# Optimization experiments

Hardware: AMD Instinct MI355X
Metric: run time of the kernel (lower is better)

## Reference

```python
import jax, jax.numpy as jnp
import numpy as np

D = 1024
D_PRE_HEAD = 128
H = 16
D_ROPE = D_PRE_HEAD // 2          # 64
DC_V = D_PRE_HEAD                 # 128
DC_KV = D_PRE_HEAD // 8           # 16
DC_Q = D // 4                     # 256
Q_HEAD_DIM = D_PRE_HEAD + D_ROPE  # 192
MEG_D = D_PRE_HEAD + DC_V         # 256
MAX_LEN = 8192
EPS = 1e-7


def rms_norm(x, w):
    x32 = x.astype(jnp.float32)
    var = jnp.mean(x32 * x32, axis=-1, keepdims=True)
    return w * (x32 * jax.lax.rsqrt(var + EPS)).astype(x.dtype)


def rope_cos_sin():
    inv_freq = 1.0 / (10000.0 ** (jnp.arange(0, D_ROPE, 2, dtype=jnp.float32) / D_ROPE))
    freqs = jnp.outer(jnp.arange(MAX_LEN, dtype=jnp.float32), inv_freq)
    emb = jnp.concatenate([freqs, freqs], axis=-1)  # [MAX_LEN, D_ROPE]
    return jnp.cos(emb), jnp.sin(emb)


def rope_reshape(x):
    # view(...,d//2,2).transpose(-1,-2).reshape == concat(even, odd) along last dim
    return jnp.concatenate([x[..., 0::2], x[..., 1::2]], axis=-1)


def rope_rotate(x):
    h = x.shape[-1] // 2
    return jnp.concatenate([-x[..., h:], x[..., :h]], axis=-1)


def setup_inputs() -> dict:
    key = jax.random.key(0)
    ks = jax.random.split(key, 12)
    B, SQ, SKV = 2, 2048, 2048
    s = 0.02
    return {
        "q_inputs": jax.random.normal(ks[0], (B, SQ, D), jnp.float32),
        "kv_input": jax.random.normal(ks[1], (B, SKV, D), jnp.float32),
        "q_pos_ids": jax.random.randint(ks[2], (B, SQ), 0, MAX_LEN),
        "kv_pos_ids": jax.random.randint(ks[3], (B, SKV), 0, MAX_LEN),
        # weights stored as [in, out] (torch Linear weight transposed)
        "Wq_down": jax.random.normal(ks[4], (D, DC_Q), jnp.float32) * s,
        "q_norm_w": jnp.ones((DC_Q,), jnp.float32),
        "Wq_up": jax.random.normal(ks[5], (DC_Q, H * Q_HEAD_DIM), jnp.float32) * s,
        "Wkv_down": jax.random.normal(ks[6], (D, DC_KV + D_ROPE), jnp.float32) * s,
        "kv_norm_w": jnp.ones((DC_KV,), jnp.float32),
        "Wkv_up": jax.random.normal(ks[7], (DC_KV, H * MEG_D), jnp.float32) * s,
        "Wout": jax.random.normal(ks[8], (H * DC_V, D), jnp.float32) * s,
    }


def reference(q_inputs, kv_input, q_pos_ids, kv_pos_ids,
              Wq_down, q_norm_w, Wq_up, Wkv_down, kv_norm_w, Wkv_up, Wout):
    B, SQ, _ = q_inputs.shape
    SKV = kv_input.shape[1]

    # query path: low-rank down -> RMSNorm -> up
    q = rms_norm(q_inputs @ Wq_down, q_norm_w) @ Wq_up
    q = q.reshape(B, SQ, H, Q_HEAD_DIM).transpose(0, 2, 1, 3)  # [B,H,SQ,192]
    q_nope, q_rope = q[..., :D_PRE_HEAD], q[..., D_PRE_HEAD:]

    # kv path: compressed latent + decoupled rope slice
    ckv_full = kv_input @ Wkv_down                              # [B,SKV,DC_KV+D_ROPE]
    c_kv, k_rope = ckv_full[..., :DC_KV], ckv_full[..., DC_KV:]
    c_kv = rms_norm(c_kv, kv_norm_w)
    kv = (c_kv @ Wkv_up).reshape(B, SKV, H, MEG_D).transpose(0, 2, 1, 3)
    k_nope, value = kv[..., :D_PRE_HEAD], kv[..., D_PRE_HEAD:]  # [B,H,SKV,128] each
    k_rope = k_rope[:, None, :, :]                              # [B,1,SKV,64]

    # RoPE with per-token position ids
    cos, sin = rope_cos_sin()
    q_cos, q_sin = cos[q_pos_ids][:, None], sin[q_pos_ids][:, None]   # [B,1,SQ,64]
    k_cos, k_sin = cos[kv_pos_ids][:, None], sin[kv_pos_ids][:, None]
    qr = rope_reshape(q_rope)
    kr = rope_reshape(k_rope)
    q_rope = qr * q_cos + rope_rotate(qr) * q_sin
    k_rope = kr * k_cos + rope_rotate(kr) * k_sin

    query = jnp.concatenate([q_nope, q_rope], axis=-1)                         # [B,H,SQ,192]
    key_t = jnp.concatenate([k_nope, jnp.broadcast_to(k_rope, (B, H, SKV, D_ROPE))], axis=-1)

    scale = 1.0 / jnp.sqrt(jnp.asarray(Q_HEAD_DIM, query.dtype))
    scores = jnp.einsum('bhqd,bhkd->bhqk', query, key_t) * scale
    attn = jax.nn.softmax(scores, axis=-1)
    out = jnp.einsum('bhqk,bhkd->bhqd', attn, value)                           # [B,H,SQ,128]
    out = out.transpose(0, 2, 1, 3).reshape(B, SQ, H * DC_V)
    return out @ Wout
```

## Files before the change

kernel.cpp:

```cpp
#include <hip/hip_runtime.h>

typedef unsigned short u16;
typedef unsigned int u32;
typedef u16 u16x4 __attribute__((ext_vector_type(4)));
typedef u16 u16x8 __attribute__((ext_vector_type(8)));
typedef u32 u32x4 __attribute__((ext_vector_type(4)));
typedef float f32x4 __attribute__((ext_vector_type(4)));
typedef __bf16 bf16x8 __attribute__((ext_vector_type(8)));

#define DEV static __device__ __forceinline__

DEV float bf2f(u16 u) { u32 v = ((u32)u) << 16; float f; __builtin_memcpy(&f, &v, 4); return f; }
DEV u16 f2bf(float f) { u32 v; __builtin_memcpy(&v, &f, 4); v += 0x7fffu + ((v >> 16) & 1u); return (u16)(v >> 16); }
DEV bf16x8 ld_frag(const u16* p) { u16x8 v = *(const u16x8*)p; return __builtin_bit_cast(bf16x8, v); }

#define LOG10000 9.210340372f

__global__ __launch_bounds__(256) void k_wtrans(const float* __restrict__ in, u16* __restrict__ out,
                                                int R, int C, int Rp) {
  __shared__ float tile[32][33];
  int c0 = blockIdx.x * 32, r0 = blockIdx.y * 32;
  int tx = threadIdx.x & 31, ty = threadIdx.x >> 5;
#pragma unroll
  for (int p = 0; p < 4; p++) {
    int r = r0 + ty + p * 8, c = c0 + tx;
    tile[ty + p * 8][tx] = (r < R && c < C) ? in[(size_t)r * C + c] : 0.f;
  }
  __syncthreads();
#pragma unroll
  for (int p = 0; p < 4; p++)
    out[(size_t)(c0 + ty + p * 8) * Rp + r0 + tx] = f2bf(tile[tx][ty + p * 8]);
}

template <int OUT_BF16>
__global__ __launch_bounds__(256) void k_gemm(const u16* __restrict__ A, const u16* __restrict__ Bt,
                                              void* __restrict__ Cv, int M, int N, int K) {
  constexpr int LSTR = 40;
  __shared__ u16 As[128 * LSTR], Bs[128 * LSTR];
  const int tid = threadIdx.x, l = tid & 63, w = tid >> 6;
  const int nwg = gridDim.x * gridDim.y;
  const int lin = blockIdx.y * gridDim.x + blockIdx.x;
  const int swzb = (lin & 7) * (nwg >> 3) + (lin >> 3);
  const int m0 = (swzb / gridDim.x) * 128, n0 = (swzb % gridDim.x) * 128;
  const int wr = (w >> 1) * 64, wc = (w & 1) * 64;
  const int lr = l & 15, lk = (l >> 4) * 8;
  const int sr = tid >> 2, sc = (tid & 3) * 8;
  f32x4 acc[4][4] = {};
  const u16* pa0 = A + (size_t)(m0 + sr) * K + sc;
  const u16* pa1 = A + (size_t)(m0 + 64 + sr) * K + sc;
  const u16* pb0 = Bt + (size_t)(n0 + sr) * K + sc;
  const u16* pb1 = Bt + (size_t)(n0 + 64 + sr) * K + sc;
  u16x8 va0 = *(const u16x8*)pa0, va1 = *(const u16x8*)pa1;
  u16x8 vb0 = *(const u16x8*)pb0, vb1 = *(const u16x8*)pb1;
  for (int k0 = 0; k0 < K; k0 += 32) {
    *(u16x8*)&As[sr * LSTR + sc] = va0;
    *(u16x8*)&As[(64 + sr) * LSTR + sc] = va1;
    *(u16x8*)&Bs[sr * LSTR + sc] = vb0;
    *(u16x8*)&Bs[(64 + sr) * LSTR + sc] = vb1;
    __syncthreads();
    if (k0 + 32 < K) {
      va0 = *(const u16x8*)(pa0 + k0 + 32);
      va1 = *(const u16x8*)(pa1 + k0 + 32);
      vb0 = *(const u16x8*)(pb0 + k0 + 32);
      vb1 = *(const u16x8*)(pb1 + k0 + 32);
    }
    bf16x8 af[4], bf[4];
#pragma unroll
    for (int i = 0; i < 4; i++) af[i] = ld_frag(&As[(wr + i * 16 + lr) * LSTR + lk]);
#pragma unroll
    for (int j = 0; j < 4; j++) bf[j] = ld_frag(&Bs[(wc + j * 16 + lr) * LSTR + lk]);
#pragma unroll
    for (int i = 0; i < 4; i++)
#pragma unroll
      for (int j = 0; j < 4; j++)
        acc[i][j] = __builtin_amdgcn_mfma_f32_16x16x32_bf16(af[i], bf[j], acc[i][j], 0, 0, 0);
    __syncthreads();
  }
#pragma unroll
  for (int i = 0; i < 4; i++)
#pragma unroll
    for (int j = 0; j < 4; j++) {
      int row = m0 + wr + i * 16 + (l >> 4) * 4;
      int col = n0 + wc + j * 16 + lr;
#pragma unroll
      for (int r = 0; r < 4; r++) {
        if (OUT_BF16) ((u16*)Cv)[(size_t)(row + r) * N + col] = f2bf(acc[i][j][r]);
        else          ((float*)Cv)[(size_t)(row + r) * N + col] = acc[i][j][r];
      }
    }
}

template <int OUT_BF16>
__global__ __launch_bounds__(256) void k_gemmh(const u16* __restrict__ A, const u16* __restrict__ Bt,
                                               void* __restrict__ Cv, int M, int N, int K) {
  constexpr int LSTR = 40;
  __shared__ u16 As[64 * LSTR], Bs[128 * LSTR];
  const int tid = threadIdx.x, l = tid & 63, w = tid >> 6;
  const int nwg = gridDim.x * gridDim.y;
  const int lin = blockIdx.y * gridDim.x + blockIdx.x;
  const int swzb = (lin & 7) * (nwg >> 3) + (lin >> 3);
  const int m0 = (swzb / gridDim.x) * 64, n0 = (swzb % gridDim.x) * 128;
  const int wr = (w >> 1) * 32, wc = (w & 1) * 64;
  const int lr = l & 15, lk = (l >> 4) * 8;
  const int sr = tid >> 2, sc = (tid & 3) * 8;
  f32x4 acc[2][4] = {};
  const u16* pa0 = A + (size_t)(m0 + sr) * K + sc;
  const u16* pb0 = Bt + (size_t)(n0 + sr) * K + sc;
  const u16* pb1 = Bt + (size_t)(n0 + 64 + sr) * K + sc;
  u16x8 va0 = *(const u16x8*)pa0;
  u16x8 vb0 = *(const u16x8*)pb0, vb1 = *(const u16x8*)pb1;
  for (int k0 = 0; k0 < K; k0 += 32) {
    *(u16x8*)&As[sr * LSTR + sc] = va0;
    *(u16x8*)&Bs[sr * LSTR + sc] = vb0;
    *(u16x8*)&Bs[(64 + sr) * LSTR + sc] = vb1;
    __syncthreads();
    if (k0 + 32 < K) {
      va0 = *(const u16x8*)(pa0 + k0 + 32);
      vb0 = *(const u16x8*)(pb0 + k0 + 32);
      vb1 = *(const u16x8*)(pb1 + k0 + 32);
    }
    bf16x8 af[2], bf[4];
#pragma unroll
    for (int i = 0; i < 2; i++) af[i] = ld_frag(&As[(wr + i * 16 + lr) * LSTR + lk]);
#pragma unroll
    for (int j = 0; j < 4; j++) bf[j] = ld_frag(&Bs[(wc + j * 16 + lr) * LSTR + lk]);
#pragma unroll
    for (int i = 0; i < 2; i++)
#pragma unroll
      for (int j = 0; j < 4; j++)
        acc[i][j] = __builtin_amdgcn_mfma_f32_16x16x32_bf16(af[i], bf[j], acc[i][j], 0, 0, 0);
    __syncthreads();
  }
#pragma unroll
  for (int i = 0; i < 2; i++)
#pragma unroll
    for (int j = 0; j < 4; j++) {
      int row = m0 + wr + i * 16 + (l >> 4) * 4;
      int col = n0 + wc + j * 16 + lr;
#pragma unroll
      for (int r = 0; r < 4; r++) {
        if (OUT_BF16) ((u16*)Cv)[(size_t)(row + r) * N + col] = f2bf(acc[i][j][r]);
        else          ((float*)Cv)[(size_t)(row + r) * N + col] = acc[i][j][r];
      }
    }
}

template <int OUT_BF16>
__global__ __launch_bounds__(256) void k_gemm64f(const float* __restrict__ A, const u16* __restrict__ Bt,
                                                 void* __restrict__ Cv, int M, int N, int K) {
  constexpr int LSTR = 40;
  __shared__ u16 As[64 * LSTR], Bs[64 * LSTR];
  const int tid = threadIdx.x, l = tid & 63, w = tid >> 6;
  const int nwg = gridDim.x * gridDim.y;
  const int lin = blockIdx.y * gridDim.x + blockIdx.x;
  const int swzb = (lin & 7) * (nwg >> 3) + (lin >> 3);
  const int m0 = (swzb / gridDim.x) * 64, n0 = (swzb % gridDim.x) * 64;
  const int wr = (w >> 1) * 32, wc = (w & 1) * 32;
  const int lr = l & 15, lk = (l >> 4) * 8;
  const int sr = tid >> 2, sc = (tid & 3) * 8;
  f32x4 acc[2][2] = {};
  const float* pa0 = A + (size_t)(m0 + sr) * K + sc;
  const u16* pb0 = Bt + (size_t)(n0 + sr) * K + sc;
  f32x4 vaa = *(const f32x4*)pa0, vab = *(const f32x4*)(pa0 + 4);
  u16x8 vb0 = *(const u16x8*)pb0;
  for (int k0 = 0; k0 < K; k0 += 32) {
    u16x8 va0 = { f2bf(vaa[0]), f2bf(vaa[1]), f2bf(vaa[2]), f2bf(vaa[3]),
                  f2bf(vab[0]), f2bf(vab[1]), f2bf(vab[2]), f2bf(vab[3]) };
    *(u16x8*)&As[sr * LSTR + sc] = va0;
    *(u16x8*)&Bs[sr * LSTR + sc] = vb0;
    __syncthreads();
    if (k0 + 32 < K) {
      vaa = *(const f32x4*)(pa0 + k0 + 32);
      vab = *(const f32x4*)(pa0 + k0 + 36);
      vb0 = *(const u16x8*)(pb0 + k0 + 32);
    }
    bf16x8 af[2], bf[2];
#pragma unroll
    for (int i = 0; i < 2; i++) af[i] = ld_frag(&As[(wr + i * 16 + lr) * LSTR + lk]);
#pragma unroll
    for (int j = 0; j < 2; j++) bf[j] = ld_frag(&Bs[(wc + j * 16 + lr) * LSTR + lk]);
#pragma unroll
    for (int i = 0; i < 2; i++)
#pragma unroll
      for (int j = 0; j < 2; j++)
        acc[i][j] = __builtin_amdgcn_mfma_f32_16x16x32_bf16(af[i], bf[j], acc[i][j], 0, 0, 0);
    __syncthreads();
  }
#pragma unroll
  for (int i = 0; i < 2; i++)
#pragma unroll
    for (int j = 0; j < 2; j++) {
      int row = m0 + wr + i * 16 + (l >> 4) * 4;
      int col = n0 + wc + j * 16 + lr;
#pragma unroll
      for (int r = 0; r < 4; r++) {
        if (OUT_BF16) ((u16*)Cv)[(size_t)(row + r) * N + col] = f2bf(acc[i][j][r]);
        else          ((float*)Cv)[(size_t)(row + r) * N + col] = acc[i][j][r];
      }
    }
}

__global__ __launch_bounds__(64) void k_kvnorm(const float* __restrict__ ckvf, const float* __restrict__ nw,
                                               const int* __restrict__ pos, u16* __restrict__ ckvn,
                                               u16* __restrict__ kropeb) {
  int row = blockIdx.x, l = threadIdx.x;
  const float* x = ckvf + (size_t)row * 128;
  float v = (l < 16) ? x[l] : 0.f;
  float ss = v * v;
  ss += __shfl_xor(ss, 1); ss += __shfl_xor(ss, 2); ss += __shfl_xor(ss, 4); ss += __shfl_xor(ss, 8);
  if (l < 16) ckvn[(size_t)row * 32 + l] = f2bf(v * rsqrtf(ss * (1.f / 16.f) + 1e-7f) * nw[l]);
  if (l >= 16 && l < 32) ckvn[(size_t)row * 32 + l] = 0;
  if (l < 32) {
    float invf = __expf(-(LOG10000 / 32.f) * (float)l);
    float ang = (float)pos[row] * invf;
    float c = cosf(ang), s = sinf(ang);
    float e = x[16 + 2 * l], o = x[17 + 2 * l];
    kropeb[(size_t)row * 64 + l]      = f2bf(e * c - o * s);
    kropeb[(size_t)row * 64 + l + 32] = f2bf(o * c + e * s);
  }
}

__global__ __launch_bounds__(256) void k_rms256(const float* __restrict__ in, const float* __restrict__ w,
                                                u16* __restrict__ out, float scale) {
  int row = blockIdx.x * 4 + (threadIdx.x >> 6);
  int l = threadIdx.x & 63;
  const float* x = in + (size_t)row * 256;
  f32x4 v = *(const f32x4*)(x + l * 4);
  float ss = v[0] * v[0] + v[1] * v[1] + v[2] * v[2] + v[3] * v[3];
#pragma unroll
  for (int m = 1; m < 64; m <<= 1) ss += __shfl_xor(ss, m);
  float rinv = rsqrtf(ss * (1.f / 256.f) + 1e-7f) * scale;
  const f32x4 wv = *(const f32x4*)(w + l * 4);
  u16x4 o = { f2bf(v[0] * rinv * wv[0]), f2bf(v[1] * rinv * wv[1]),
              f2bf(v[2] * rinv * wv[2]), f2bf(v[3] * rinv * wv[3]) };
  *(u16x4*)(out + (size_t)row * 256 + l * 4) = o;
}

__global__ __launch_bounds__(256) void k_qrope(u16* __restrict__ q, const int* __restrict__ pos) {
  __shared__ float cs[32], sn[32];
  int bs = blockIdx.x, tid = threadIdx.x;
  if (tid < 32) {
    float invf = __expf(-(LOG10000 / 32.f) * (float)tid);
    float ang = (float)pos[bs] * invf;
    cs[tid] = cosf(ang); sn[tid] = sinf(ang);
  }
  __syncthreads();
  u16* base = q + (size_t)bs * 3072;
  int h0 = tid >> 5, p0 = tid & 31;
  int h1 = h0 + 8, p1 = p0;
  u16* r0p = base + h0 * 192 + 128;
  u16* r1p = base + h1 * 192 + 128;
  float e0 = bf2f(r0p[2 * p0]), o0 = bf2f(r0p[2 * p0 + 1]);
  float e1 = bf2f(r1p[2 * p1]), o1 = bf2f(r1p[2 * p1 + 1]);
  __syncthreads();
  r0p[p0]      = f2bf(e0 * cs[p0] - o0 * sn[p0]);
  r0p[p0 + 32] = f2bf(o0 * cs[p0] + e0 * sn[p0]);
  r1p[p1]      = f2bf(e1 * cs[p1] - o1 * sn[p1]);
  r1p[p1 + 32] = f2bf(o1 * cs[p1] + e1 * sn[p1]);
}

__global__ __launch_bounds__(256) void k_vt(const u16* __restrict__ Ckv, u16* __restrict__ VT) {
  __shared__ u16 tile[64][72];
  int bh = blockIdx.z, b = bh >> 4, h = bh & 15;
  int d0 = blockIdx.x * 64, s0 = blockIdx.y * 64;
  int tid = threadIdx.x;
#pragma unroll
  for (int p = 0; p < 2; p++) {
    int c = tid + p * 256;
    int r = c >> 3, cc = (c & 7) * 8;
    *(u16x8*)&tile[r][cc] =
        *(const u16x8*)&Ckv[((size_t)(b * 2048 + s0 + r)) * 4096 + h * 256 + 128 + d0 + cc];
  }
  __syncthreads();
#pragma unroll
  for (int p = 0; p < 2; p++) {
    int c = tid + p * 256;
    int d = c >> 3, ss = (c & 7) * 8;
    u16x8 v = { tile[ss][d],     tile[ss + 1][d], tile[ss + 2][d], tile[ss + 3][d],
                tile[ss + 4][d], tile[ss + 5][d], tile[ss + 6][d], tile[ss + 7][d] };
    *(u16x8*)&VT[((size_t)bh * 128 + d0 + d) * 2048 + s0 + ss] = v;
  }
}

__global__ __launch_bounds__(512, 2) void k_attn(const u16* __restrict__ Qp, const u16* __restrict__ Ckv,
                                                 const u16* __restrict__ kropeb, const u16* __restrict__ VT,
                                                 u16* __restrict__ AO) {
  __shared__ u16 Ks[64 * 192];
  __shared__ u16 Vs[128 * 64];
  const int tid = threadIdx.x, l = tid & 63, w = tid >> 6;
  const int lr = l & 15, g = l >> 4, lk = g * 8;
  const int bid = blockIdx.x, bh = bid & 31, qt = bid >> 5;
  const int b = bh >> 4, hh = bh & 15;
  const int m0 = qt * 128;
  const u32 swz = (u32)(lr & 7) << 3;

  bf16x8 qa[6];
  {
    const u16* qrow = Qp + (size_t)(b * 2048 + m0 + w * 16 + lr) * 3072 + hh * 192;
#pragma unroll
    for (int kk = 0; kk < 6; kk++) qa[kk] = ld_frag(qrow + kk * 32 + lk);
  }

  const u16* kptr[3]; int kstep[3]; u32 klds[3];
#pragma unroll
  for (int p = 0; p < 3; p++) {
    int c2 = tid + p * 512;
    int r = c2 / 24, cc = c2 - r * 24;
    klds[p] = (u32)(r * 192 + cc * 8) ^ ((u32)(r & 7) << 3);
    if (cc < 16) { kptr[p] = Ckv + ((size_t)(b * 2048 + r)) * 4096 + hh * 256 + cc * 8; kstep[p] = 64 * 4096; }
    else         { kptr[p] = kropeb + ((size_t)(b * 2048 + r)) * 64 + (cc - 16) * 8;    kstep[p] = 64 * 64; }
  }
  const u16* vptr[2]; u32 vlds[2];
#pragma unroll
  for (int p = 0; p < 2; p++) {
    int c2 = tid + p * 512;
    int d = c2 >> 3, cc = c2 & 7;
    vlds[p] = (u32)(d * 64 + cc * 8) ^ ((u32)(d & 7) << 3);
    vptr[p] = VT + ((size_t)bh * 128 + d) * 2048 + cc * 8;
  }
  u16x8 kreg[3], vreg[2];
#pragma unroll
  for (int p = 0; p < 3; p++) { kreg[p] = *(const u16x8*)kptr[p]; kptr[p] += kstep[p]; }
#pragma unroll
  for (int p = 0; p < 2; p++) { vreg[p] = *(const u16x8*)vptr[p]; vptr[p] += 64; }

  f32x4 oacc[8] = {};
  float lsum = 0.f;
  const int srcA = lr + ((l & 16) << 1);
  const int srcB = srcA + 16;
  const bool hi = (l & 32) != 0;

  for (int t = 0; t < 32; t++) {
#pragma unroll
    for (int p = 0; p < 3; p++) *(u16x8*)&Ks[klds[p]] = kreg[p];
#pragma unroll
    for (int p = 0; p < 2; p++) *(u16x8*)&Vs[vlds[p]] = vreg[p];
    __syncthreads();
    if (t + 1 < 32) {
#pragma unroll
      for (int p = 0; p < 3; p++) { kreg[p] = *(const u16x8*)kptr[p]; kptr[p] += kstep[p]; }
#pragma unroll
      for (int p = 0; p < 2; p++) { vreg[p] = *(const u16x8*)vptr[p]; vptr[p] += 64; }
    }
    f32x4 sacc[4] = {};
    __builtin_amdgcn_s_setprio(1);
#pragma unroll
    for (int n = 0; n < 4; n++)
#pragma unroll
      for (int kk = 0; kk < 6; kk++)
        sacc[n] = __builtin_amdgcn_mfma_f32_16x16x32_bf16(
            ld_frag(&Ks[(u32)((n * 16 + lr) * 192 + kk * 32 + lk) ^ swz]), qa[kk], sacc[n], 0, 0, 0);
    __builtin_amdgcn_s_setprio(0);
    u32 pw[4][2];
#pragma unroll
    for (int n = 0; n < 4; n++) {
      float p0 = __expf(sacc[n][0]), p1 = __expf(sacc[n][1]),
            p2 = __expf(sacc[n][2]), p3 = __expf(sacc[n][3]);
      lsum += (p0 + p1) + (p2 + p3);
      pw[n][0] = (u32)f2bf(p0) | ((u32)f2bf(p1) << 16);
      pw[n][1] = (u32)f2bf(p2) | ((u32)f2bf(p3) << 16);
    }
    u32 pa32[2][4];
#pragma unroll
    for (int kk2 = 0; kk2 < 2; kk2++) {
      u32 t0a = __shfl(pw[2 * kk2][0], srcA), t1a = __shfl(pw[2 * kk2 + 1][0], srcA);
      u32 t0b = __shfl(pw[2 * kk2][1], srcA), t1b = __shfl(pw[2 * kk2 + 1][1], srcA);
      u32 t0c = __shfl(pw[2 * kk2][0], srcB), t1c = __shfl(pw[2 * kk2 + 1][0], srcB);
      u32 t0d = __shfl(pw[2 * kk2][1], srcB), t1d = __shfl(pw[2 * kk2 + 1][1], srcB);
      pa32[kk2][0] = hi ? t1a : t0a;
      pa32[kk2][1] = hi ? t1b : t0b;
      pa32[kk2][2] = hi ? t1c : t0c;
      pa32[kk2][3] = hi ? t1d : t0d;
    }
    __builtin_amdgcn_s_setprio(1);
#pragma unroll
    for (int kk2 = 0; kk2 < 2; kk2++) {
      u32x4 pv = { pa32[kk2][0], pa32[kk2][1], pa32[kk2][2], pa32[kk2][3] };
      bf16x8 paf = __builtin_bit_cast(bf16x8, pv);
#pragma unroll
      for (int n2 = 0; n2 < 8; n2++)
        oacc[n2] = __builtin_amdgcn_mfma_f32_16x16x32_bf16(
            paf, ld_frag(&Vs[(u32)((n2 * 16 + lr) * 64 + kk2 * 32 + lk) ^ swz]), oacc[n2], 0, 0, 0);
    }
    __builtin_amdgcn_s_setprio(0);
    __syncthreads();
  }
  float s = lsum;
  s += __shfl_xor(s, 16);
  s += __shfl_xor(s, 32);
  float rl = 1.f / s;
  float rlv[4];
#pragma unroll
  for (int r = 0; r < 4; r++) rlv[r] = __shfl(rl, g * 4 + r);
#pragma unroll
  for (int n2 = 0; n2 < 8; n2++)
#pragma unroll
    for (int r = 0; r < 4; r++) {
      int row = m0 + w * 16 + g * 4 + r;
      AO[((size_t)(b * 2048 + row) * 16 + hh) * 128 + n2 * 16 + lr] = f2bf(oacc[n2][r] * rlv[r]);
    }
}

extern "C" void kernel_launch(void* const* d_in, const int* in_sizes, int n_in,
                              void* d_out, int out_size, void* d_ws, size_t ws_size,
                              hipStream_t stream) {
  const float* q_in  = (const float*)d_in[0];
  const float* kv_in = (const float*)d_in[1];
  const int*   qpos  = (const int*)d_in[2];
  const int*   kpos  = (const int*)d_in[3];
  const float* Wqd   = (const float*)d_in[4];
  const float* qnw   = (const float*)d_in[5];
  const float* Wqu   = (const float*)d_in[6];
  const float* Wkvd  = (const float*)d_in[7];
  const float* kvnw  = (const float*)d_in[8];
  const float* Wkvu  = (const float*)d_in[9];
  const float* Wo    = (const float*)d_in[10];
  float* out = (float*)d_out;
  char* ws = (char*)d_ws;
  size_t off = 0;
  auto alloc = [&](size_t bytes) -> void* {
    void* p = ws + off; off += (bytes + 255) & ~(size_t)255; return p;
  };
  u16*   WqdT   = (u16*)alloc(256ull * 1024 * 2);
  u16*   WquT   = (u16*)alloc(3072ull * 256 * 2);
  u16*   WkvdT  = (u16*)alloc(128ull * 1024 * 2);
  u16*   WkvuT  = (u16*)alloc(4096ull * 32 * 2);
  u16*   WoT    = (u16*)alloc(1024ull * 2048 * 2);
  float* ckvf   = (float*)alloc(4096ull * 128 * 4);
  u16*   ckvn   = (u16*)alloc(4096ull * 32 * 2);
  u16*   kropeb = (u16*)alloc(4096ull * 64 * 2);
  u16*   Ckv    = (u16*)alloc(4096ull * 4096 * 2);
  u16*   VTb    = (u16*)alloc(32ull * 128 * 2048 * 2);
  float* cq     = (float*)alloc(4096ull * 256 * 4);
  u16*   cqn    = (u16*)alloc(4096ull * 256 * 2);
  u16*   qproj  = (u16*)alloc(4096ull * 3072 * 2);
  u16*   AOb    = (u16*)alloc(4096ull * 2048 * 2);
  (void)in_sizes; (void)n_in; (void)out_size; (void)ws_size;

  k_wtrans<<<dim3(8, 32), 256, 0, stream>>>(Wqd, WqdT, 1024, 256, 1024);
  k_wtrans<<<dim3(96, 8), 256, 0, stream>>>(Wqu, WquT, 256, 3072, 256);
  k_wtrans<<<dim3(4, 32), 256, 0, stream>>>(Wkvd, WkvdT, 1024, 80, 1024);
  k_wtrans<<<dim3(128, 1), 256, 0, stream>>>(Wkvu, WkvuT, 16, 4096, 32);
  k_wtrans<<<dim3(32, 64), 256, 0, stream>>>(Wo, WoT, 2048, 1024, 2048);
  k_gemm64f<0><<<dim3(2, 64), 256, 0, stream>>>(kv_in, WkvdT, ckvf, 4096, 128, 1024);
  k_kvnorm<<<4096, 64, 0, stream>>>(ckvf, kvnw, kpos, ckvn, kropeb);
  k_gemm<1><<<dim3(32, 32), 256, 0, stream>>>(ckvn, WkvuT, Ckv, 4096, 4096, 32);
  k_vt<<<dim3(2, 32, 32), 256, 0, stream>>>(Ckv, VTb);
  k_gemm64f<0><<<dim3(4, 64), 256, 0, stream>>>(q_in, WqdT, cq, 4096, 256, 1024);
  k_rms256<<<1024, 256, 0, stream>>>(cq, qnw, cqn, 0.07216878364870322f);
  k_gemm<1><<<dim3(24, 32), 256, 0, stream>>>(cqn, WquT, qproj, 4096, 3072, 256);
  k_qrope<<<4096, 256, 0, stream>>>(qproj, qpos);
  k_attn<<<512, 512, 0, stream>>>(qproj, Ckv, kropeb, VTb, AOb);
  k_gemmh<0><<<dim3(8, 64), 256, 0, stream>>>(AOb, WoT, out, 4096, 1024, 2048);
}
```

Measured before the change: 259.3 us.

## Fuse V transpose into KV up-projection GEMM and double-buffer attention LDS

Adds a KV up-projection GEMM that writes K-nope columns to Ckv and writes the value columns straight into the transposed VT layout, removing the separate k_vt transpose kernel and one pass over the V data. The attention kernel now double-buffers its K/V shared-memory tiles and prefetches two tiles ahead, so the store of the next tile overlaps compute on the current one. LDS use per block doubles to about 80KB, which may limit the two-blocks-per-CU occupancy target. The VT stores are 8-byte strided writes rather than coalesced rows.

```diff
diff --git a/kernel.cpp b/kernel.cpp
--- a/kernel.cpp
+++ b/kernel.cpp
@@ -90,6 +90,77 @@
     }
 }
 
+__global__ __launch_bounds__(256) void k_gemm_kv(const u16* __restrict__ A, const u16* __restrict__ Bt,
+                                                 u16* __restrict__ Ckv, u16* __restrict__ VT,
+                                                 int M, int N, int K) {
+  constexpr int LSTR = 40;
+  __shared__ u16 As[128 * LSTR], Bs[128 * LSTR];
+  const int tid = threadIdx.x, l = tid & 63, w = tid >> 6;
+  const int nwg = gridDim.x * gridDim.y;
+  const int lin = blockIdx.y * gridDim.x + blockIdx.x;
+  const int swzb = (lin & 7) * (nwg >> 3) + (lin >> 3);
+  const int m0 = (swzb / gridDim.x) * 128, n0 = (swzb % gridDim.x) * 128;
+  const int wr = (w >> 1) * 64, wc = (w & 1) * 64;
+  const int lr = l & 15, lk = (l >> 4) * 8;
+  const int sr = tid >> 2, sc = (tid & 3) * 8;
+  f32x4 acc[4][4] = {};
+  const u16* pa0 = A + (size_t)(m0 + sr) * K + sc;
+  const u16* pa1 = A + (size_t)(m0 + 64 + sr) * K + sc;
+  const u16* pb0 = Bt + (size_t)(n0 + sr) * K + sc;
+  const u16* pb1 = Bt + (size_t)(n0 + 64 + sr) * K + sc;
+  u16x8 va0 = *(const u16x8*)pa0, va1 = *(const u16x8*)pa1;
+  u16x8 vb0 = *(const u16x8*)pb0, vb1 = *(const u16x8*)pb1;
+  for (int k0 = 0; k0 < K; k0 += 32) {
+    *(u16x8*)&As[sr * LSTR + sc] = va0;
+    *(u16x8*)&As[(64 + sr) * LSTR + sc] = va1;
+    *(u16x8*)&Bs[sr * LSTR + sc] = vb0;
+    *(u16x8*)&Bs[(64 + sr) * LSTR + sc] = vb1;
+    __syncthreads();
+    if (k0 + 32 < K) {
+      va0 = *(const u16x8*)(pa0 + k0 + 32);
+      va1 = *(const u16x8*)(pa1 + k0 + 32);
+      vb0 = *(const u16x8*)(pb0 + k0 + 32);
+      vb1 = *(const u16x8*)(pb1 + k0 + 32);
+    }
+    bf16x8 af[4], bf[4];
+#pragma unroll
+    for (int i = 0; i < 4; i++) af[i] = ld_frag(&As[(wr + i * 16 + lr) * LSTR + lk]);
+#pragma unroll
+    for (int j = 0; j < 4; j++) bf[j] = ld_frag(&Bs[(wc + j * 16 + lr) * LSTR + lk]);
+#pragma unroll
+    for (int i = 0; i < 4; i++)
+#pragma unroll
+      for (int j = 0; j < 4; j++)
+        acc[i][j] = __builtin_amdgcn_mfma_f32_16x16x32_bf16(af[i], bf[j], acc[i][j], 0, 0, 0);
+    __syncthreads();
+  }
+  if ((n0 & 255) < 128) {
+#pragma unroll
+    for (int i = 0; i < 4; i++)
+#pragma unroll
+      for (int j = 0; j < 4; j++) {
+        int row = m0 + wr + i * 16 + (l >> 4) * 4;
+        int col = n0 + wc + j * 16 + lr;
+#pragma unroll
+        for (int r = 0; r < 4; r++)
+          Ckv[(size_t)(row + r) * N + col] = f2bf(acc[i][j][r]);
+      }
+  } else {
+#pragma unroll
+    for (int i = 0; i < 4; i++)
+#pragma unroll
+      for (int j = 0; j < 4; j++) {
+        int row = m0 + wr + i * 16 + (l >> 4) * 4;
+        int col = n0 + wc + j * 16 + lr;
+        int bb = row >> 11, srow = row & 2047;
+        int hh2 = col >> 8, d = col & 127;
+        u16x4 pk = { f2bf(acc[i][j][0]), f2bf(acc[i][j][1]),
+                     f2bf(acc[i][j][2]), f2bf(acc[i][j][3]) };
+        *(u16x4*)&VT[((size_t)(bb * 16 + hh2) * 128 + d) * 2048 + srow] = pk;
+      }
+  }
+}
+
 template <int OUT_BF16>
 __global__ __launch_bounds__(256) void k_gemmh(const u16* __restrict__ A, const u16* __restrict__ Bt,
                                                void* __restrict__ Cv, int M, int N, int K) {
@@ -259,34 +330,12 @@
   r1p[p1 + 32] = f2bf(o1 * cs[p1] + e1 * sn[p1]);
 }
 
-__global__ __launch_bounds__(256) void k_vt(const u16* __restrict__ Ckv, u16* __restrict__ VT) {
-  __shared__ u16 tile[64][72];
-  int bh = blockIdx.z, b = bh >> 4, h = bh & 15;
-  int d0 = blockIdx.x * 64, s0 = blockIdx.y * 64;
-  int tid = threadIdx.x;
-#pragma unroll
-  for (int p = 0; p < 2; p++) {
-    int c = tid + p * 256;
-    int r = c >> 3, cc = (c & 7) * 8;
-    *(u16x8*)&tile[r][cc] =
-        *(const u16x8*)&Ckv[((size_t)(b * 2048 + s0 + r)) * 4096 + h * 256 + 128 + d0 + cc];
-  }
-  __syncthreads();
-#pragma unroll
-  for (int p = 0; p < 2; p++) {
-    int c = tid + p * 256;
-    int d = c >> 3, ss = (c & 7) * 8;
-    u16x8 v = { tile[ss][d],     tile[ss + 1][d], tile[ss + 2][d], tile[ss + 3][d],
-                tile[ss + 4][d], tile[ss + 5][d], tile[ss + 6][d], tile[ss + 7][d] };
-    *(u16x8*)&VT[((size_t)bh * 128 + d0 + d) * 2048 + s0 + ss] = v;
-  }
-}
-
 __global__ __launch_bounds__(512, 2) void k_attn(const u16* __restrict__ Qp, const u16* __restrict__ Ckv,
                                                  const u16* __restrict__ kropeb, const u16* __restrict__ VT,
                                                  u16* __restrict__ AO) {
-  __shared__ u16 Ks[64 * 192];
-  __shared__ u16 Vs[128 * 64];
+  constexpr u32 KSZ = 64 * 192, VSZ = 128 * 64;
+  __shared__ u16 Ks[2 * KSZ];
+  __shared__ u16 Vs[2 * VSZ];
   const int tid = threadIdx.x, l = tid & 63, w = tid >> 6;
   const int lr = l & 15, g = l >> 4, lk = g * 8;
   const int bid = blockIdx.x, bh = bid & 31, qt = bid >> 5;
@@ -323,6 +372,15 @@
   for (int p = 0; p < 3; p++) { kreg[p] = *(const u16x8*)kptr[p]; kptr[p] += kstep[p]; }
 #pragma unroll
   for (int p = 0; p < 2; p++) { vreg[p] = *(const u16x8*)vptr[p]; vptr[p] += 64; }
+#pragma unroll
+  for (int p = 0; p < 3; p++) *(u16x8*)&Ks[klds[p]] = kreg[p];
+#pragma unroll
+  for (int p = 0; p < 2; p++) *(u16x8*)&Vs[vlds[p]] = vreg[p];
+#pragma unroll
+  for (int p = 0; p < 3; p++) { kreg[p] = *(const u16x8*)kptr[p]; kptr[p] += kstep[p]; }
+#pragma unroll
+  for (int p = 0; p < 2; p++) { vreg[p] = *(const u16x8*)vptr[p]; vptr[p] += 64; }
+  __syncthreads();
 
   f32x4 oacc[8] = {};
   float lsum = 0.f;
@@ -331,12 +389,15 @@
   const bool hi = (l & 32) != 0;
 
   for (int t = 0; t < 32; t++) {
-#pragma unroll
-    for (int p = 0; p < 3; p++) *(u16x8*)&Ks[klds[p]] = kreg[p];
-#pragma unroll
-    for (int p = 0; p < 2; p++) *(u16x8*)&Vs[vlds[p]] = vreg[p];
-    __syncthreads();
+    const u32 curK = (u32)(t & 1) * KSZ, curV = (u32)(t & 1) * VSZ;
+    const u32 nxtK = curK ^ KSZ, nxtV = curV ^ VSZ;
     if (t + 1 < 32) {
+#pragma unroll
+      for (int p = 0; p < 3; p++) *(u16x8*)&Ks[nxtK + klds[p]] = kreg[p];
+#pragma unroll
+      for (int p = 0; p < 2; p++) *(u16x8*)&Vs[nxtV + vlds[p]] = vreg[p];
+    }
+    if (t + 2 < 32) {
 #pragma unroll
       for (int p = 0; p < 3; p++) { kreg[p] = *(const u16x8*)kptr[p]; kptr[p] += kstep[p]; }
 #pragma unroll
@@ -349,7 +410,7 @@
 #pragma unroll
       for (int kk = 0; kk < 6; kk++)
         sacc[n] = __builtin_amdgcn_mfma_f32_16x16x32_bf16(
-            ld_frag(&Ks[(u32)((n * 16 + lr) * 192 + kk * 32 + lk) ^ swz]), qa[kk], sacc[n], 0, 0, 0);
+            ld_frag(&Ks[curK + ((u32)((n * 16 + lr) * 192 + kk * 32 + lk) ^ swz)]), qa[kk], sacc[n], 0, 0, 0);
     __builtin_amdgcn_s_setprio(0);
     u32 pw[4][2];
 #pragma unroll
@@ -380,7 +441,7 @@
 #pragma unroll
       for (int n2 = 0; n2 < 8; n2++)
         oacc[n2] = __builtin_amdgcn_mfma_f32_16x16x32_bf16(
-            paf, ld_frag(&Vs[(u32)((n2 * 16 + lr) * 64 + kk2 * 32 + lk) ^ swz]), oacc[n2], 0, 0, 0);
+            paf, ld_frag(&Vs[curV + ((u32)((n2 * 16 + lr) * 64 + kk2 * 32 + lk) ^ swz)]), oacc[n2], 0, 0, 0);
     }
     __builtin_amdgcn_s_setprio(0);
     __syncthreads();
@@ -444,8 +505,7 @@
   k_wtrans<<<dim3(32, 64), 256, 0, stream>>>(Wo, WoT, 2048, 1024, 2048);
   k_gemm64f<0><<<dim3(2, 64), 256, 0, stream>>>(kv_in, WkvdT, ckvf, 4096, 128, 1024);
   k_kvnorm<<<4096, 64, 0, stream>>>(ckvf, kvnw, kpos, ckvn, kropeb);
-  k_gemm<1><<<dim3(32, 32), 256, 0, stream>>>(ckvn, WkvuT, Ckv, 4096, 4096, 32);
-  k_vt<<<dim3(2, 32, 32), 256, 0, stream>>>(Ckv, VTb);
+  k_gemm_kv<<<dim3(32, 32), 256, 0, stream>>>(ckvn, WkvuT, Ckv, VTb, 4096, 4096, 32);
   k_gemm64f<0><<<dim3(4, 64), 256, 0, stream>>>(q_in, WqdT, cq, 4096, 256, 1024);
   k_rms256<<<1024, 256, 0, stream>>>(cq, qnw, cqn, 0.07216878364870322f);
   k_gemm<1><<<dim3(24, 32), 256, 0, stream>>>(cqn, WquT, qproj, 4096, 3072, 256);
```

New measurement: 258.4 us. No clear change (-0.3%).

## Batch launches into merged kernels and fuse V transpose into KV up-projection

Applied to the files above, without the earlier changes.

Merges the five weight-transpose launches into one grid, the two down-projection GEMMs into one, the two norm kernels into one, and the two up-projection GEMMs into one, cutting launch count and tail effects. The KV up-projection epilogue now writes the value half directly in transposed layout, removing the separate V-transpose kernel and its extra read/write pass. The attention kernel uses native bf16 conversions for packing probabilities. The transposed V writes are strided 8-byte stores, which may coalesce worse than the old tiled transpose.

```diff
diff --git a/kernel.cpp b/kernel.cpp
--- a/kernel.cpp
+++ b/kernel.cpp
@@ -7,6 +7,7 @@
 typedef u32 u32x4 __attribute__((ext_vector_type(4)));
 typedef float f32x4 __attribute__((ext_vector_type(4)));
 typedef __bf16 bf16x8 __attribute__((ext_vector_type(8)));
+typedef __bf16 bf16x2 __attribute__((ext_vector_type(2)));
 
 #define DEV static __device__ __forceinline__
 
@@ -16,10 +17,20 @@
 
 #define LOG10000 9.210340372f
 
-__global__ __launch_bounds__(256) void k_wtrans(const float* __restrict__ in, u16* __restrict__ out,
-                                                int R, int C, int Rp) {
+__global__ __launch_bounds__(256) void k_wtrans5(
+    const float* __restrict__ Wqd, const float* __restrict__ Wqu, const float* __restrict__ Wkvd,
+    const float* __restrict__ Wkvu, const float* __restrict__ Wo,
+    u16* __restrict__ WqdT, u16* __restrict__ WquT, u16* __restrict__ WkvdT,
+    u16* __restrict__ WkvuT, u16* __restrict__ WoT) {
   __shared__ float tile[32][33];
-  int c0 = blockIdx.x * 32, r0 = blockIdx.y * 32;
+  int id = blockIdx.x;
+  const float* in; u16* out; int R, C, Rp, bx, by;
+  if (id < 256)       { in = Wqd;  out = WqdT;  R = 1024; C = 256;  Rp = 1024; bx = id & 7;  by = id >> 3; }
+  else if (id < 1024) { id -= 256;  in = Wqu;  out = WquT;  R = 256;  C = 3072; Rp = 256;  bx = id % 96; by = id / 96; }
+  else if (id < 1152) { id -= 1024; in = Wkvd; out = WkvdT; R = 1024; C = 80;   Rp = 1024; bx = id & 3;  by = id >> 2; }
+  else if (id < 1280) { id -= 1152; in = Wkvu; out = WkvuT; R = 16;   C = 4096; Rp = 32;   bx = id;      by = 0; }
+  else                { id -= 1280; in = Wo;   out = WoT;   R = 2048; C = 1024; Rp = 2048; bx = id & 31; by = id >> 5; }
+  int c0 = bx * 32, r0 = by * 32;
   int tx = threadIdx.x & 31, ty = threadIdx.x >> 5;
 #pragma unroll
   for (int p = 0; p < 4; p++) {
@@ -32,16 +43,112 @@
     out[(size_t)(c0 + ty + p * 8) * Rp + r0 + tx] = f2bf(tile[tx][ty + p * 8]);
 }
 
-template <int OUT_BF16>
-__global__ __launch_bounds__(256) void k_gemm(const u16* __restrict__ A, const u16* __restrict__ Bt,
-                                              void* __restrict__ Cv, int M, int N, int K) {
+DEV void gemm64f_body(int m0, int n0, const float* __restrict__ A, const u16* __restrict__ Bt,
+                      float* __restrict__ C, int N, int K, int tid, u16* As, u16* Bs) {
   constexpr int LSTR = 40;
-  __shared__ u16 As[128 * LSTR], Bs[128 * LSTR];
-  const int tid = threadIdx.x, l = tid & 63, w = tid >> 6;
-  const int nwg = gridDim.x * gridDim.y;
-  const int lin = blockIdx.y * gridDim.x + blockIdx.x;
-  const int swzb = (lin & 7) * (nwg >> 3) + (lin >> 3);
-  const int m0 = (swzb / gridDim.x) * 128, n0 = (swzb % gridDim.x) * 128;
+  const int l = tid & 63, w = tid >> 6;
+  const int wr = (w >> 1) * 32, wc = (w & 1) * 32;
+  const int lr = l & 15, lk = (l >> 4) * 8;
+  const int sr = tid >> 2, sc = (tid & 3) * 8;
+  f32x4 acc[2][2] = {};
+  const float* pa0 = A + (size_t)(m0 + sr) * K + sc;
+  const u16* pb0 = Bt + (size_t)(n0 + sr) * K + sc;
+  f32x4 vaa = *(const f32x4*)pa0, vab = *(const f32x4*)(pa0 + 4);
+  u16x8 vb0 = *(const u16x8*)pb0;
+  for (int k0 = 0; k0 < K; k0 += 32) {
+    u16x8 va0 = { f2bf(vaa[0]), f2bf(vaa[1]), f2bf(vaa[2]), f2bf(vaa[3]),
+                  f2bf(vab[0]), f2bf(vab[1]), f2bf(vab[2]), f2bf(vab[3]) };
+    *(u16x8*)&As[sr * LSTR + sc] = va0;
+    *(u16x8*)&Bs[sr * LSTR + sc] = vb0;
+    __syncthreads();
+    if (k0 + 32 < K) {
+      vaa = *(const f32x4*)(pa0 + k0 + 32);
+      vab = *(const f32x4*)(pa0 + k0 + 36);
+      vb0 = *(const u16x8*)(pb0 + k0 + 32);
+    }
+    bf16x8 af[2], bf[2];
+#pragma unroll
+    for (int i = 0; i < 2; i++) af[i] = ld_frag(&As[(wr + i * 16 + lr) * LSTR + lk]);
+#pragma unroll
+    for (int j = 0; j < 2; j++) bf[j] = ld_frag(&Bs[(wc + j * 16 + lr) * LSTR + lk]);
+#pragma unroll
+    for (int i = 0; i < 2; i++)
+#pragma unroll
+      for (int j = 0; j < 2; j++)
+        acc[i][j] = __builtin_amdgcn_mfma_f32_16x16x32_bf16(af[i], bf[j], acc[i][j], 0, 0, 0);
+    __syncthreads();
+  }
+#pragma unroll
+  for (int i = 0; i < 2; i++)
+#pragma unroll
+    for (int j = 0; j < 2; j++) {
+      int row = m0 + wr + i * 16 + (l >> 4) * 4;
+      int col = n0 + wc + j * 16 + lr;
+#pragma unroll
+      for (int r = 0; r < 4; r++)
+        C[(size_t)(row + r) * N + col] = acc[i][j][r];
+    }
+}
+
+__global__ __launch_bounds__(256) void k_downs(const float* __restrict__ q_in, const float* __restrict__ kv_in,
+                                               const u16* __restrict__ WqdT, const u16* __restrict__ WkvdT,
+                                               float* __restrict__ cq, float* __restrict__ ckvf) {
+  __shared__ u16 As[64 * 40], Bs[64 * 40];
+  int id = blockIdx.x, tid = threadIdx.x;
+  if (id < 128) {
+    int swzb = (id & 7) * 16 + (id >> 3);
+    gemm64f_body((swzb >> 1) * 64, (swzb & 1) * 64, kv_in, WkvdT, ckvf, 128, 1024, tid, As, Bs);
+  } else {
+    int lin = id - 128;
+    int swzb = (lin & 7) * 32 + (lin >> 3);
+    gemm64f_body((swzb >> 2) * 64, (swzb & 3) * 64, q_in, WqdT, cq, 256, 1024, tid, As, Bs);
+  }
+}
+
+__global__ __launch_bounds__(256) void k_norms(const float* __restrict__ ckvf, const float* __restrict__ kvnw,
+                                               const int* __restrict__ kpos, u16* __restrict__ ckvn,
+                                               u16* __restrict__ kropeb,
+                                               const float* __restrict__ cq, const float* __restrict__ qnw,
+                                               u16* __restrict__ cqn, float scale) {
+  int id = blockIdx.x, tid = threadIdx.x;
+  int l = tid & 63;
+  if (id < 1024) {
+    int row = id * 4 + (tid >> 6);
+    const float* x = ckvf + (size_t)row * 128;
+    float v = (l < 16) ? x[l] : 0.f;
+    float ss = v * v;
+    ss += __shfl_xor(ss, 1); ss += __shfl_xor(ss, 2); ss += __shfl_xor(ss, 4); ss += __shfl_xor(ss, 8);
+    if (l < 16) ckvn[(size_t)row * 32 + l] = f2bf(v * rsqrtf(ss * (1.f / 16.f) + 1e-7f) * kvnw[l]);
+    if (l >= 16 && l < 32) ckvn[(size_t)row * 32 + l] = 0;
+    if (l < 32) {
+      float invf = __expf(-(LOG10000 / 32.f) * (float)l);
+      float ang = (float)kpos[row] * invf;
+      float c = cosf(ang), s = sinf(ang);
+      float e = x[16 + 2 * l], o = x[17 + 2 * l];
+      kropeb[(size_t)row * 64 + l]      = f2bf(e * c - o * s);
+      kropeb[(size_t)row * 64 + l + 32] = f2bf(o * c + e * s);
+    }
+  } else {
+    int row = (id - 1024) * 4 + (tid >> 6);
+    const float* x = cq + (size_t)row * 256;
+    f32x4 v = *(const f32x4*)(x + l * 4);
+    float ss = v[0] * v[0] + v[1] * v[1] + v[2] * v[2] + v[3] * v[3];
+#pragma unroll
+    for (int m = 1; m < 64; m <<= 1) ss += __shfl_xor(ss, m);
+    float rinv = rsqrtf(ss * (1.f / 256.f) + 1e-7f) * scale;
+    const f32x4 wv = *(const f32x4*)(qnw + l * 4);
+    u16x4 o = { f2bf(v[0] * rinv * wv[0]), f2bf(v[1] * rinv * wv[1]),
+                f2bf(v[2] * rinv * wv[2]), f2bf(v[3] * rinv * wv[3]) };
+    *(u16x4*)(cqn + (size_t)row * 256 + l * 4) = o;
+  }
+}
+
+template <int MODE>
+DEV void gemm128_body(int m0, int n0, const u16* __restrict__ A, const u16* __restrict__ Bt,
+                      u16* __restrict__ C0, u16* __restrict__ C1, int N, int K, int tid,
+                      u16* As, u16* Bs) {
+  constexpr int LSTR = 40;
+  const int l = tid & 63, w = tid >> 6;
   const int wr = (w >> 1) * 64, wc = (w & 1) * 64;
   const int lr = l & 15, lk = (l >> 4) * 8;
   const int sr = tid >> 2, sc = (tid & 3) * 8;
@@ -76,23 +183,51 @@
         acc[i][j] = __builtin_amdgcn_mfma_f32_16x16x32_bf16(af[i], bf[j], acc[i][j], 0, 0, 0);
     __syncthreads();
   }
-#pragma unroll
-  for (int i = 0; i < 4; i++)
-#pragma unroll
-    for (int j = 0; j < 4; j++) {
-      int row = m0 + wr + i * 16 + (l >> 4) * 4;
-      int col = n0 + wc + j * 16 + lr;
-#pragma unroll
-      for (int r = 0; r < 4; r++) {
-        if (OUT_BF16) ((u16*)Cv)[(size_t)(row + r) * N + col] = f2bf(acc[i][j][r]);
-        else          ((float*)Cv)[(size_t)(row + r) * N + col] = acc[i][j][r];
+  if (MODE == 0 || (n0 & 255) < 128) {
+#pragma unroll
+    for (int i = 0; i < 4; i++)
+#pragma unroll
+      for (int j = 0; j < 4; j++) {
+        int row = m0 + wr + i * 16 + (l >> 4) * 4;
+        int col = n0 + wc + j * 16 + lr;
+#pragma unroll
+        for (int r = 0; r < 4; r++)
+          C0[(size_t)(row + r) * N + col] = f2bf(acc[i][j][r]);
       }
-    }
-}
-
-template <int OUT_BF16>
+  } else {
+#pragma unroll
+    for (int i = 0; i < 4; i++)
+#pragma unroll
+      for (int j = 0; j < 4; j++) {
+        int row = m0 + wr + i * 16 + (l >> 4) * 4;
+        int col = n0 + wc + j * 16 + lr;
+        int bb = row >> 11, srow = row & 2047;
+        int hh2 = col >> 8, d = col & 127;
+        u16x4 pk = { f2bf(acc[i][j][0]), f2bf(acc[i][j][1]),
+                     f2bf(acc[i][j][2]), f2bf(acc[i][j][3]) };
+        *(u16x4*)&C1[((size_t)(bb * 16 + hh2) * 128 + d) * 2048 + srow] = pk;
+      }
+  }
+}
+
+__global__ __launch_bounds__(256) void k_ups(const u16* __restrict__ ckvn, const u16* __restrict__ WkvuT,
+                                             u16* __restrict__ Ckv, u16* __restrict__ VTb,
+                                             const u16* __restrict__ cqn, const u16* __restrict__ WquT,
+                                             u16* __restrict__ qproj) {
+  __shared__ u16 As[128 * 40], Bs[128 * 40];
+  int id = blockIdx.x, tid = threadIdx.x;
+  if (id < 1024) {
+    int swzb = (id & 7) * 128 + (id >> 3);
+    gemm128_body<1>((swzb >> 5) * 128, (swzb & 31) * 128, ckvn, WkvuT, Ckv, VTb, 4096, 32, tid, As, Bs);
+  } else {
+    int lin = id - 1024;
+    int swzb = (lin & 7) * 96 + (lin >> 3);
+    gemm128_body<0>((swzb / 24) * 128, (swzb % 24) * 128, cqn, WquT, qproj, nullptr, 3072, 256, tid, As, Bs);
+  }
+}
+
 __global__ __launch_bounds__(256) void k_gemmh(const u16* __restrict__ A, const u16* __restrict__ Bt,
-                                               void* __restrict__ Cv, int M, int N, int K) {
+                                               float* __restrict__ Cv, int M, int N, int K) {
   constexpr int LSTR = 40;
   __shared__ u16 As[64 * LSTR], Bs[128 * LSTR];
   const int tid = threadIdx.x, l = tid & 63, w = tid >> 6;
@@ -138,102 +273,9 @@
       int row = m0 + wr + i * 16 + (l >> 4) * 4;
       int col = n0 + wc + j * 16 + lr;
 #pragma unroll
-      for (int r = 0; r < 4; r++) {
-        if (OUT_BF16) ((u16*)Cv)[(size_t)(row + r) * N + col] = f2bf(acc[i][j][r]);
-        else          ((float*)Cv)[(size_t)(row + r) * N + col] = acc[i][j][r];
-      }
-    }
-}
-
-template <int OUT_BF16>
-__global__ __launch_bounds__(256) void k_gemm64f(const float* __restrict__ A, const u16* __restrict__ Bt,
-                                                 void* __restrict__ Cv, int M, int N, int K) {
-  constexpr int LSTR = 40;
-  __shared__ u16 As[64 * LSTR], Bs[64 * LSTR];
-  const int tid = threadIdx.x, l = tid & 63, w = tid >> 6;
-  const int nwg = gridDim.x * gridDim.y;
-  const int lin = blockIdx.y * gridDim.x + blockIdx.x;
-  const int swzb = (lin & 7) * (nwg >> 3) + (lin >> 3);
-  const int m0 = (swzb / gridDim.x) * 64, n0 = (swzb % gridDim.x) * 64;
-  const int wr = (w >> 1) * 32, wc = (w & 1) * 32;
-  const int lr = l & 15, lk = (l >> 4) * 8;
-  const int sr = tid >> 2, sc = (tid & 3) * 8;
-  f32x4 acc[2][2] = {};
-  const float* pa0 = A + (size_t)(m0 + sr) * K + sc;
-  const u16* pb0 = Bt + (size_t)(n0 + sr) * K + sc;
-  f32x4 vaa = *(const f32x4*)pa0, vab = *(const f32x4*)(pa0 + 4);
-  u16x8 vb0 = *(const u16x8*)pb0;
-  for (int k0 = 0; k0 < K; k0 += 32) {
-    u16x8 va0 = { f2bf(vaa[0]), f2bf(vaa[1]), f2bf(vaa[2]), f2bf(vaa[3]),
-                  f2bf(vab[0]), f2bf(vab[1]), f2bf(vab[2]), f2bf(vab[3]) };
-    *(u16x8*)&As[sr * LSTR + sc] = va0;
-    *(u16x8*)&Bs[sr * LSTR + sc] = vb0;
-    __syncthreads();
-    if (k0 + 32 < K) {
-      vaa = *(const f32x4*)(pa0 + k0 + 32);
-      vab = *(const f32x4*)(pa0 + k0 + 36);
-      vb0 = *(const u16x8*)(pb0 + k0 + 32);
-    }
-    bf16x8 af[2], bf[2];
-#pragma unroll
-    for (int i = 0; i < 2; i++) af[i] = ld_frag(&As[(wr + i * 16 + lr) * LSTR + lk]);
-#pragma unroll
-    for (int j = 0; j < 2; j++) bf[j] = ld_frag(&Bs[(wc + j * 16 + lr) * LSTR + lk]);
-#pragma unroll
-    for (int i = 0; i < 2; i++)
-#pragma unroll
-      for (int j = 0; j < 2; j++)
-        acc[i][j] = __builtin_amdgcn_mfma_f32_16x16x32_bf16(af[i], bf[j], acc[i][j], 0, 0, 0);
-    __syncthreads();
-  }
-#pragma unroll
-  for (int i = 0; i < 2; i++)
-#pragma unroll
-    for (int j = 0; j < 2; j++) {
-      int row = m0 + wr + i * 16 + (l >> 4) * 4;
-      int col = n0 + wc + j * 16 + lr;
-#pragma unroll
-      for (int r = 0; r < 4; r++) {
-        if (OUT_BF16) ((u16*)Cv)[(size_t)(row + r) * N + col] = f2bf(acc[i][j][r]);
-        else          ((float*)Cv)[(size_t)(row + r) * N + col] = acc[i][j][r];
-      }
-    }
-}
-
-__global__ __launch_bounds__(64) void k_kvnorm(const float* __restrict__ ckvf, const float* __restrict__ nw,
-                                               const int* __restrict__ pos, u16* __restrict__ ckvn,
-                                               u16* __restrict__ kropeb) {
-  int row = blockIdx.x, l = threadIdx.x;
-  const float* x = ckvf + (size_t)row * 128;
-  float v = (l < 16) ? x[l] : 0.f;
-  float ss = v * v;
-  ss += __shfl_xor(ss, 1); ss += __shfl_xor(ss, 2); ss += __shfl_xor(ss, 4); ss += __shfl_xor(ss, 8);
-  if (l < 16) ckvn[(size_t)row * 32 + l] = f2bf(v * rsqrtf(ss * (1.f / 16.f) + 1e-7f) * nw[l]);
-  if (l >= 16 && l < 32) ckvn[(size_t)row * 32 + l] = 0;
-  if (l < 32) {
-    float invf = __expf(-(LOG10000 / 32.f) * (float)l);
-    float ang = (float)pos[row] * invf;
-    float c = cosf(ang), s = sinf(ang);
-    float e = x[16 + 2 * l], o = x[17 + 2 * l];
-    kropeb[(size_t)row * 64 + l]      = f2bf(e * c - o * s);
-    kropeb[(size_t)row * 64 + l + 32] = f2bf(o * c + e * s);
-  }
-}
-
-__global__ __launch_bounds__(256) void k_rms256(const float* __restrict__ in, const float* __restrict__ w,
-                                                u16* __restrict__ out, float scale) {
-  int row = blockIdx.x * 4 + (threadIdx.x >> 6);
-  int l = threadIdx.x & 63;
-  const float* x = in + (size_t)row * 256;
-  f32x4 v = *(const f32x4*)(x + l * 4);
-  float ss = v[0] * v[0] + v[1] * v[1] + v[2] * v[2] + v[3] * v[3];
-#pragma unroll
-  for (int m = 1; m < 64; m <<= 1) ss += __shfl_xor(ss, m);
-  float rinv = rsqrtf(ss * (1.f / 256.f) + 1e-7f) * scale;
-  const f32x4 wv = *(const f32x4*)(w + l * 4);
-  u16x4 o = { f2bf(v[0] * rinv * wv[0]), f2bf(v[1] * rinv * wv[1]),
-              f2bf(v[2] * rinv * wv[2]), f2bf(v[3] * rinv * wv[3]) };
-  *(u16x4*)(out + (size_t)row * 256 + l * 4) = o;
+      for (int r = 0; r < 4; r++)
+        Cv[(size_t)(row + r) * N + col] = acc[i][j][r];
+    }
 }
 
 __global__ __launch_bounds__(256) void k_qrope(u16* __restrict__ q, const int* __restrict__ pos) {
@@ -259,29 +301,6 @@
   r1p[p1 + 32] = f2bf(o1 * cs[p1] + e1 * sn[p1]);
 }
 
-__global__ __launch_bounds__(256) void k_vt(const u16* __restrict__ Ckv, u16* __restrict__ VT) {
-  __shared__ u16 tile[64][72];
-  int bh = blockIdx.z, b = bh >> 4, h = bh & 15;
-  int d0 = blockIdx.x * 64, s0 = blockIdx.y * 64;
-  int tid = threadIdx.x;
-#pragma unroll
-  for (int p = 0; p < 2; p++) {
-    int c = tid + p * 256;
-    int r = c >> 3, cc = (c & 7) * 8;
-    *(u16x8*)&tile[r][cc] =
-        *(const u16x8*)&Ckv[((size_t)(b * 2048 + s0 + r)) * 4096 + h * 256 + 128 + d0 + cc];
-  }
-  __syncthreads();
-#pragma unroll
-  for (int p = 0; p < 2; p++) {
-    int c = tid + p * 256;
-    int d = c >> 3, ss = (c & 7) * 8;
-    u16x8 v = { tile[ss][d],     tile[ss + 1][d], tile[ss + 2][d], tile[ss + 3][d],
-                tile[ss + 4][d], tile[ss + 5][d], tile[ss + 6][d], tile[ss + 7][d] };
-    *(u16x8*)&VT[((size_t)bh * 128 + d0 + d) * 2048 + s0 + ss] = v;
-  }
-}
-
 __global__ __launch_bounds__(512, 2) void k_attn(const u16* __restrict__ Qp, const u16* __restrict__ Ckv,
                                                  const u16* __restrict__ kropeb, const u16* __restrict__ VT,
                                                  u16* __restrict__ AO) {
@@ -357,8 +376,10 @@
       float p0 = __expf(sacc[n][0]), p1 = __expf(sacc[n][1]),
             p2 = __expf(sacc[n][2]), p3 = __expf(sacc[n][3]);
       lsum += (p0 + p1) + (p2 + p3);
-      pw[n][0] = (u32)f2bf(p0) | ((u32)f2bf(p1) << 16);
-      pw[n][1] = (u32)f2bf(p2) | ((u32)f2bf(p3) << 16);
+      bf16x2 a01 = { (__bf16)p0, (__bf16)p1 };
+      bf16x2 a23 = { (__bf16)p2, (__bf16)p3 };
+      pw[n][0] = __builtin_bit_cast(u32, a01);
+      pw[n][1] = __builtin_bit_cast(u32, a23);
     }
     u32 pa32[2][4];
 #pragma unroll
@@ -437,19 +458,11 @@
   u16*   AOb    = (u16*)alloc(4096ull * 2048 * 2);
   (void)in_sizes; (void)n_in; (void)out_size; (void)ws_size;
 
-  k_wtrans<<<dim3(8, 32), 256, 0, stream>>>(Wqd, WqdT, 1024, 256, 1024);
-  k_wtrans<<<dim3(96, 8), 256, 0, stream>>>(Wqu, WquT, 256, 3072, 256);
-  k_wtrans<<<dim3(4, 32), 256, 0, stream>>>(Wkvd, WkvdT, 1024, 80, 1024);
-  k_wtrans<<<dim3(128, 1), 256, 0, stream>>>(Wkvu, WkvuT, 16, 4096, 32);
-  k_wtrans<<<dim3(32, 64), 256, 0, stream>>>(Wo, WoT, 2048, 1024, 2048);
-  k_gemm64f<0><<<dim3(2, 64), 256, 0, stream>>>(kv_in, WkvdT, ckvf, 4096, 128, 1024);
-  k_kvnorm<<<4096, 64, 0, stream>>>(ckvf, kvnw, kpos, ckvn, kropeb);
-  k_gemm<1><<<dim3(32, 32), 256, 0, stream>>>(ckvn, WkvuT, Ckv, 4096, 4096, 32);
-  k_vt<<<dim3(2, 32, 32), 256, 0, stream>>>(Ckv, VTb);
-  k_gemm64f<0><<<dim3(4, 64), 256, 0, stream>>>(q_in, WqdT, cq, 4096, 256, 1024);
-  k_rms256<<<1024, 256, 0, stream>>>(cq, qnw, cqn, 0.07216878364870322f);
-  k_gemm<1><<<dim3(24, 32), 256, 0, stream>>>(cqn, WquT, qproj, 4096, 3072, 256);
+  k_wtrans5<<<3328, 256, 0, stream>>>(Wqd, Wqu, Wkvd, Wkvu, Wo, WqdT, WquT, WkvdT, WkvuT, WoT);
+  k_downs<<<384, 256, 0, stream>>>(q_in, kv_in, WqdT, WkvdT, cq, ckvf);
+  k_norms<<<2048, 256, 0, stream>>>(ckvf, kvnw, kpos, ckvn, kropeb, cq, qnw, cqn, 0.07216878364870322f);
+  k_ups<<<1792, 256, 0, stream>>>(ckvn, WkvuT, Ckv, VTb, cqn, WquT, qproj);
   k_qrope<<<4096, 256, 0, stream>>>(qproj, qpos);
   k_attn<<<512, 512, 0, stream>>>(qproj, Ckv, kropeb, VTb, AOb);
-  k_gemmh<0><<<dim3(8, 64), 256, 0, stream>>>(AOb, WoT, out, 4096, 1024, 2048);
-}
+  k_gemmh<<<dim3(8, 64), 256, 0, stream>>>(AOb, WoT, out, 4096, 1024, 2048);
+}
```

Measured after the change: 213.1 us. -17.8%, faster.
